# Kernel optimization log

Measured on AMD Instinct MI355X. Metric: run time of the kernel, lower is better.

The kernel has to match this reference:

```python
import jax, jax.numpy as jnp
import numpy as np

B, N, DIN, DH = 16, 512, 128, 256
NEG = -9.0e15  # matches -9000000000000000.0 in torch source


def _xavier(key, fan_in, fan_out):
    lim = float(np.sqrt(6.0 / (fan_in + fan_out)))
    return jax.random.uniform(key, (fan_in, fan_out), jnp.float32, -lim, lim)


def _l2n(x, eps=1e-12):
    # torch F.normalize: x / max(||x||, eps)
    return x / jnp.maximum(jnp.linalg.norm(x, axis=-1, keepdims=True), eps)


def _prelu(x, a):
    return jnp.where(x >= 0, x, a * x)


def setup_inputs() -> dict:
    key = jax.random.key(0)
    ks = jax.random.split(key, 12)
    seq = jax.random.normal(ks[0], (B, N, DIN), jnp.float32)
    # sparse-ish nonnegative adjacency with self loops, row-normalized
    u = jax.random.uniform(ks[1], (B, N, N), jnp.float32)
    a = jnp.where(u < 0.1, u, 0.0) + jnp.eye(N, dtype=jnp.float32)[None]
    adj = a / a.sum(-1, keepdims=True)
    # dense diffusion matrix, row-normalized
    d = jax.random.uniform(ks[2], (B, N, N), jnp.float32)
    diff = d / d.sum(-1, keepdims=True)
    # dropout keep-mask for F.dropout(p=0.1, training=True)
    keep = jax.random.bernoulli(ks[3], 0.9, (B, N, N)).astype(jnp.float32)
    drop_mask = keep / 0.9
    return {
        "seq": seq, "adj": adj, "diff": diff, "drop_mask": drop_mask,
        "fc1_w": _xavier(ks[4], DIN, DH),
        "q_w": _xavier(ks[5], DH, DH),
        "k_w": _xavier(ks[6], DH, DH),
        "v_w1": _xavier(ks[7], DH, DH),
        "v_w2": _xavier(ks[8], DH, DH),
        "fc2_w": _xavier(ks[9], DIN, DH),
        "bias1": jnp.zeros((DH,), jnp.float32),
        "bias2": jnp.zeros((DH,), jnp.float32),
        "prelu1_a": jnp.float32(0.25),
        "prelu2_a": jnp.float32(0.25),
        "v_prelu_a": jnp.float32(0.25),
    }


def reference(seq, adj, diff, drop_mask, fc1_w, q_w, k_w, v_w1, v_w2,
              fc2_w, bias1, bias2, prelu1_a, prelu2_a, v_prelu_a):
    # ---- GCN1 (attention branch) ----
    fts = seq @ fc1_w                                   # [B,N,H]
    out = jnp.einsum('bmn,bnh->bmh', adj, fts)          # adj aggregation
    q = _l2n(out @ q_w)
    k = _l2n(out @ k_w)
    scores = jax.lax.stop_gradient(jnp.einsum('bmd,bnd->bmn', q, k))  # .detach()
    div_loss = jnp.mean(jnp.sum((q - k) ** 2, axis=-1))
    att = jnp.where(adj > 0, scores, NEG)
    att = jax.nn.softmax(att, axis=-1) * drop_mask      # dropout(p=0.1)
    agg = jnp.einsum('bmn,bnh->bmh', att, out)
    v = _prelu(agg @ v_w1, v_prelu_a) @ v_w2 + bias1
    h1 = _prelu(v, prelu1_a)
    # ---- GCN2 (plain branch) ----
    h2 = _prelu(jnp.einsum('bmn,bnh->bmh', diff, seq @ fc2_w) + bias2, prelu2_a)
    # ---- Readout ----
    c1 = jnp.mean(h1, axis=1)                           # [B,H]
    c2 = jnp.mean(h2, axis=1)
    # ---- DIS ----
    n1 = _l2n(h1).reshape(B * N, DH)
    n2 = _l2n(h2).reshape(B * N, DH)
    node_logits = n1 @ n2.T                             # [B*N, B*N]
    graph_logits = _l2n(c1) @ _l2n(c2).T                # [B, B]
    return node_logits, graph_logits, div_loss
```

## Files before the change

### kernel.cpp

```cpp
#include <hip/hip_runtime.h>
#include <hip/hip_bf16.h>


using bf16x8 = __attribute__((ext_vector_type(8))) short;
using f32x4  = __attribute__((ext_vector_type(4))) float;

__device__ __forceinline__ unsigned short f2b(float f) {
    union { float f; unsigned int u; } x; x.f = f;
    unsigned int r = x.u + 0x7FFFu + ((x.u >> 16) & 1u);
    return (unsigned short)(r >> 16);
}
__device__ __forceinline__ void gload_lds16(const void* g, void* l) {
    __builtin_amdgcn_global_load_lds(
        (const __attribute__((address_space(1))) void*)g,
        (__attribute__((address_space(3))) void*)l, 16, 0, 0);
}

__global__ __launch_bounds__(256) void prep(
    const float* __restrict__ seq, const float* __restrict__ adj,
    const float* __restrict__ diff,
    const float* __restrict__ fc1, const float* __restrict__ fc2,
    const float* __restrict__ qw,  const float* __restrict__ kw,
    const float* __restrict__ v1,  const float* __restrict__ v2,
    unsigned short* __restrict__ seq_bf, unsigned short* __restrict__ adj_bf,
    unsigned short* __restrict__ diff_bf,
    unsigned short* fc1T, unsigned short* fc2T, unsigned short* qwT,
    unsigned short* kwT,  unsigned short* v1T,  unsigned short* v2T)
{
    __shared__ float t[32][33];
    const int bid = blockIdx.x, tid = threadIdx.x;
    if (bid < 9216) {
        long i = (long)bid * 256 + tid;
        const float* src; unsigned short* dst; long off;
        if (i < 262144)       { src = seq;  dst = seq_bf;  off = i; }
        else if (i < 1310720) { src = adj;  dst = adj_bf;  off = i - 262144; }
        else                  { src = diff; dst = diff_bf; off = i - 1310720; }
        float4 v = reinterpret_cast<const float4*>(src)[off];
        ushort4 o; o.x = f2b(v.x); o.y = f2b(v.y); o.z = f2b(v.z); o.w = f2b(v.w);
        reinterpret_cast<ushort4*>(dst)[off] = o;
        return;
    }
    const int r = bid - 9216;
    const int z = r >> 6;
    const float* in; unsigned short* op; int R;
    if      (z == 0) { in = fc1; op = fc1T; R = 128; }
    else if (z == 1) { in = fc2; op = fc2T; R = 128; }
    else if (z == 2) { in = qw;  op = qwT;  R = 256; }
    else if (z == 3) { in = kw;  op = kwT;  R = 256; }
    else if (z == 4) { in = v1;  op = v1T;  R = 256; }
    else             { in = v2;  op = v2T;  R = 256; }
    const int c0 = (r & 7) * 32, r0 = ((r >> 3) & 7) * 32;
    if (r0 >= R) return;
    const int x = tid & 31, y = tid >> 5;
    for (int i = 0; i < 32; i += 8) t[y + i][x] = in[(long)(r0 + y + i) * 256 + c0 + x];
    __syncthreads();
    for (int i = 0; i < 32; i += 8)
        op[(long)(c0 + y + i) * R + r0 + x] = f2b(t[x][y + i]);
}

#define BN 128
#define BK 64

template<int TBM, bool WF, bool WB, bool SWZ>
__global__ __launch_bounds__(256) void gemm_nt(
    const unsigned short* __restrict__ A, const unsigned short* __restrict__ Bt,
    float* __restrict__ Cf, unsigned short* __restrict__ Cb,
    int M, int Nn, int K, int lda, int ldb, int ldc,
    long sA, long sB, long sC)
{
    constexpr int MI = TBM / 32;
    __shared__ unsigned short As[TBM][BK];
    __shared__ unsigned short Bs[BN][BK];
    const int b = blockIdx.z;
    A  += (long)b * sA;
    Bt += (long)b * sB;
    const long cbase = (long)b * sC;

    int tx, ty;
    if (SWZ) {
        int bid = blockIdx.y * gridDim.x + blockIdx.x;
        int nwg = gridDim.x * gridDim.y;
        int cpx = nwg >> 3;
        int s = (bid & 7) * cpx + (bid >> 3);
        tx = s % gridDim.x; ty = s / gridDim.x;
    } else { tx = blockIdx.x; ty = blockIdx.y; }
    const int tile_m = ty * TBM;
    const int tile_n = tx * BN;

    const int tid  = threadIdx.x;
    const int lane = tid & 63;
    const int wave = tid >> 6;
    const int wm = (wave >> 1) * (TBM / 2);
    const int wn = (wave & 1) << 6;
    const int lrow = lane >> 3;
    const int lcol = (lane & 7) << 3;

    f32x4 acc[MI][4] = {};

    for (int k0 = 0; k0 < K; k0 += BK) {
        #pragma unroll
        for (int i = 0; i < TBM / 32; ++i) {
            const int rb = (i * 4 + wave) * 8;
            gload_lds16(A + (long)(tile_m + rb + lrow) * lda + k0 + lcol, &As[rb][0]);
        }
        #pragma unroll
        for (int i = 0; i < 4; ++i) {
            const int rb = (i * 4 + wave) * 8;
            gload_lds16(Bt + (long)(tile_n + rb + lrow) * ldb + k0 + lcol, &Bs[rb][0]);
        }
        __syncthreads();
        #pragma unroll
        for (int ks = 0; ks < 2; ++ks) {
            const int kk = ks * 32 + ((lane >> 4) << 3);
            bf16x8 af[MI], bq[4];
            #pragma unroll
            for (int mi = 0; mi < MI; ++mi)
                af[mi] = *reinterpret_cast<const bf16x8*>(&As[wm + (lane & 15) + mi * 16][kk]);
            #pragma unroll
            for (int ni = 0; ni < 4; ++ni)
                bq[ni] = *reinterpret_cast<const bf16x8*>(&Bs[wn + (lane & 15) + ni * 16][kk]);
            #pragma unroll
            for (int mi = 0; mi < MI; ++mi)
                #pragma unroll
                for (int ni = 0; ni < 4; ++ni)
                    acc[mi][ni] = __builtin_amdgcn_mfma_f32_16x16x32_bf16(
                        af[mi], bq[ni], acc[mi][ni], 0, 0, 0);
        }
        __syncthreads();
    }

    const int c0 = lane & 15;
    const int r0 = (lane >> 4) << 2;
    #pragma unroll
    for (int ni = 0; ni < 4; ++ni) {
        const int col = tile_n + wn + ni * 16 + c0;
        #pragma unroll
        for (int mi = 0; mi < MI; ++mi) {
            const int row0 = tile_m + wm + mi * 16 + r0;
            if (WF) {
                #pragma unroll
                for (int j = 0; j < 4; ++j)
                    Cf[cbase + (long)(row0 + j) * ldc + col] = acc[mi][ni][j];
            }
            if (WB) {
                #pragma unroll
                for (int j = 0; j < 4; ++j)
                    Cb[cbase + (long)(row0 + j) * ldc + col] = f2b(acc[mi][ni][j]);
            }
        }
    }
}

__global__ __launch_bounds__(256) void gcn1qk(
    const unsigned short* __restrict__ adj_bf,
    const unsigned short* __restrict__ ftsT,
    const unsigned short* __restrict__ qkT,
    unsigned short* __restrict__ outT,
    unsigned short* __restrict__ q_bf,
    unsigned short* __restrict__ k_bf)
{
    __shared__ unsigned char smem[73984];
    unsigned short* Ot  = (unsigned short*)smem;
    unsigned short* As  = (unsigned short*)(smem + 8448);
    unsigned short* Bs  = (unsigned short*)(smem + 10496);
    unsigned short* Bs2 = (unsigned short*)(smem + 8448);
    __shared__ float sred[16][4];

    const int b  = blockIdx.y;
    const int m0 = blockIdx.x << 4;
    const unsigned short* ap = adj_bf + ((long)b * 512 + m0) * 512;

    const int tid = threadIdx.x, lane = tid & 63, wave = tid >> 6;
    const int lrow = lane >> 3, lcol = (lane & 7) << 3;
    const int hi = lane >> 4, c0 = lane & 15, r0 = hi << 2;

    {
        const int wn = wave << 6;
        f32x4 acc[4] = {};
        for (int k0 = 0; k0 < 512; k0 += 64) {
            if (wave < 2)
                gload_lds16(ap + (long)(wave * 8 + lrow) * 512 + k0 + lcol, &As[wave * 8 * 64]);
            #pragma unroll
            for (int i = 0; i < 8; ++i) {
                const int rb = (i * 4 + wave) * 8;
                gload_lds16(ftsT + (long)(rb + lrow) * 8192 + b * 512 + k0 + lcol, &Bs[rb * 64]);
            }
            __syncthreads();
            #pragma unroll
            for (int ks = 0; ks < 2; ++ks) {
                const int kk = ks * 32 + (hi << 3);
                bf16x8 af = *reinterpret_cast<const bf16x8*>(&As[c0 * 64 + kk]);
                #pragma unroll
                for (int ni = 0; ni < 4; ++ni) {
                    bf16x8 bq = *reinterpret_cast<const bf16x8*>(&Bs[(wn + ni * 16 + c0) * 64 + kk]);
                    acc[ni] = __builtin_amdgcn_mfma_f32_16x16x32_bf16(af, bq, acc[ni], 0, 0, 0);
                }
            }
            __syncthreads();
        }
        #pragma unroll
        for (int ni = 0; ni < 4; ++ni) {
            const int col = wn + ni * 16 + c0;
            ushort4 o;
            unsigned short* e = (unsigned short*)&o;
            #pragma unroll
            for (int j = 0; j < 4; ++j) {
                unsigned short v = f2b(acc[ni][j]);
                e[j] = v;
                Ot[(r0 + j) * 264 + col] = v;
            }
            *reinterpret_cast<ushort4*>(
                &outT[(long)b * 131072 + (long)col * 512 + m0 + r0]) = o;
        }
    }

    {
        const int wn = wave << 7;
        f32x4 acc[8] = {};
        for (int k0 = 0; k0 < 256; k0 += 64) {
            #pragma unroll
            for (int i = 0; i < 16; ++i) {
                const int rb = (i * 4 + wave) * 8;
                gload_lds16(qkT + (long)(rb + lrow) * 256 + k0 + lcol, &Bs2[rb * 64]);
            }
            __syncthreads();
            #pragma unroll
            for (int ks = 0; ks < 2; ++ks) {
                const int kk = ks * 32 + (hi << 3);
                bf16x8 af = *reinterpret_cast<const bf16x8*>(&Ot[c0 * 264 + k0 + kk]);
                #pragma unroll
                for (int ni = 0; ni < 8; ++ni) {
                    bf16x8 bq = *reinterpret_cast<const bf16x8*>(&Bs2[(wn + ni * 16 + c0) * 64 + kk]);
                    acc[ni] = __builtin_amdgcn_mfma_f32_16x16x32_bf16(af, bq, acc[ni], 0, 0, 0);
                }
            }
            __syncthreads();
        }
        float rs[4] = {};
        #pragma unroll
        for (int ni = 0; ni < 8; ++ni)
            #pragma unroll
            for (int j = 0; j < 4; ++j) { float x = acc[ni][j]; rs[j] += x * x; }
        #pragma unroll
        for (int o = 1; o <= 8; o <<= 1)
            #pragma unroll
            for (int j = 0; j < 4; ++j) rs[j] += __shfl_xor(rs[j], o);
        if (c0 == 0) {
            #pragma unroll
            for (int j = 0; j < 4; ++j) sred[r0 + j][wave] = rs[j];
        }
        __syncthreads();
        float inv[4];
        #pragma unroll
        for (int j = 0; j < 4; ++j) {
            const int rr = r0 + j;
            float sq = sred[rr][0] + sred[rr][1];
            float sk = sred[rr][2] + sred[rr][3];
            inv[j] = 1.f / fmaxf(sqrtf(wave < 2 ? sq : sk), 1e-12f);
        }
        #pragma unroll
        for (int ni = 0; ni < 8; ++ni)
            #pragma unroll
            for (int j = 0; j < 4; ++j) {
                const long rowg = (long)b * 512 + m0 + r0 + j;
                const int col = wn + ni * 16 + c0;
                unsigned short v = f2b(acc[ni][j] * inv[j]);
                if (wave < 2) q_bf[rowg * 256 + col] = v;
                else          k_bf[rowg * 256 + col - 256] = v;
            }
    }
}

__global__ __launch_bounds__(256) void attmlp_h2(
    const unsigned short* __restrict__ q_bf,
    const unsigned short* __restrict__ k_bf,
    const unsigned short* __restrict__ adj_bf,
    const float* __restrict__ drop,
    const unsigned short* __restrict__ outT,
    const unsigned short* __restrict__ w1T,
    const unsigned short* __restrict__ w2T,
    const float* __restrict__ bias1,
    const float* __restrict__ av, const float* __restrict__ a1,
    unsigned short* __restrict__ n1,
    float* __restrict__ psum1,
    float* __restrict__ rowpart,
    const unsigned short* __restrict__ diff_bf,
    const unsigned short* __restrict__ fts2T,
    const float* __restrict__ bias2, const float* __restrict__ a2,
    unsigned short* __restrict__ n2,
    float* __restrict__ psum2)
{
    __shared__ unsigned char smem[69632];
    __shared__ float redm[32][4], reds[32][4];

    const int idx = blockIdx.x >> 1;
    const int tid = threadIdx.x, lane = tid & 63, wave = tid >> 6;
    const int lrow = lane >> 3, lcol = (lane & 7) << 3;
    const int hi = lane >> 4, c0 = lane & 15, r0 = hi << 2;

    if (blockIdx.x & 1) {
        unsigned short* As  = (unsigned short*)smem;
        unsigned short* Bs  = (unsigned short*)(smem + 4096);
        unsigned short* Pls = (unsigned short*)smem;
        unsigned short* Bs2 = (unsigned short*)(smem + 34816);
        unsigned short* T   = (unsigned short*)smem;
        unsigned short* Bs3 = (unsigned short*)(smem + 16896);

        const int b  = idx >> 4;
        const int m0 = (idx & 15) << 5;
        const unsigned short* qp = q_bf + (long)b * 131072 + (long)m0 * 256;
        const unsigned short* kp = k_bf + (long)b * 131072;
        const unsigned short* ot = outT + (long)b * 131072;
        const unsigned short* ap = adj_bf + ((long)b * 512 + m0) * 512;
        const float*          dp = drop   + ((long)b * 512 + m0) * 512;

        {
            const int wn = wave << 7;
            f32x4 acc[2][8] = {};
            for (int k0 = 0; k0 < 256; k0 += 64) {
                gload_lds16(qp + (long)(wave * 8 + lrow) * 256 + k0 + lcol, &As[wave * 8 * 64]);
                #pragma unroll
                for (int i = 0; i < 16; ++i) {
                    const int rb = (i * 4 + wave) * 8;
                    gload_lds16(kp + (long)(rb + lrow) * 256 + k0 + lcol, &Bs[rb * 64]);
                }
                __syncthreads();
                #pragma unroll
                for (int ks = 0; ks < 2; ++ks) {
                    const int kk = ks * 32 + (hi << 3);
                    bf16x8 af[2], bq[8];
                    #pragma unroll
                    for (int mi = 0; mi < 2; ++mi)
                        af[mi] = *reinterpret_cast<const bf16x8*>(&As[(mi * 16 + c0) * 64 + kk]);
                    #pragma unroll
                    for (int ni = 0; ni < 8; ++ni)
                        bq[ni] = *reinterpret_cast<const bf16x8*>(&Bs[(wn + ni * 16 + c0) * 64 + kk]);
                    #pragma unroll
                    for (int mi = 0; mi < 2; ++mi)
                        #pragma unroll
                        for (int ni = 0; ni < 8; ++ni)
                            acc[mi][ni] = __builtin_amdgcn_mfma_f32_16x16x32_bf16(
                                af[mi], bq[ni], acc[mi][ni], 0, 0, 0);
                }
                __syncthreads();
            }

            float rmax[2][4];
            #pragma unroll
            for (int mi = 0; mi < 2; ++mi)
                #pragma unroll
                for (int j = 0; j < 4; ++j) rmax[mi][j] = -3.0e38f;
            #pragma unroll
            for (int mi = 0; mi < 2; ++mi)
                #pragma unroll
                for (int ni = 0; ni < 8; ++ni)
                    #pragma unroll
                    for (int j = 0; j < 4; ++j) {
                        const int rowl = mi * 16 + r0 + j;
                        const int col  = wn + ni * 16 + c0;
                        float s = acc[mi][ni][j];
                        if (col == m0 + rowl)
                            rowpart[(long)b * 512 + m0 + rowl] = 2.f - 2.f * s;
                        bool m = ap[(long)rowl * 512 + col] != 0;
                        s = m ? s : -3.0e38f;
                        acc[mi][ni][j] = s;
                        rmax[mi][j] = fmaxf(rmax[mi][j], s);
                    }
            #pragma unroll
            for (int o = 1; o <= 8; o <<= 1)
                #pragma unroll
                for (int mi = 0; mi < 2; ++mi)
                    #pragma unroll
                    for (int j = 0; j < 4; ++j)
                        rmax[mi][j] = fmaxf(rmax[mi][j], __shfl_xor(rmax[mi][j], o));
            if (c0 == 0) {
                #pragma unroll
                for (int mi = 0; mi < 2; ++mi)
                    #pragma unroll
                    for (int j = 0; j < 4; ++j) redm[mi * 16 + r0 + j][wave] = rmax[mi][j];
            }
            __syncthreads();
            float mx[2][4], rsum[2][4];
            #pragma unroll
            for (int mi = 0; mi < 2; ++mi)
                #pragma unroll
                for (int j = 0; j < 4; ++j) {
                    const int rr = mi * 16 + r0 + j;
                    mx[mi][j] = fmaxf(fmaxf(redm[rr][0], redm[rr][1]),
                                      fmaxf(redm[rr][2], redm[rr][3]));
                    rsum[mi][j] = 0.f;
                }
            #pragma unroll
            for (int mi = 0; mi < 2; ++mi)
                #pragma unroll
                for (int ni = 0; ni < 8; ++ni)
                    #pragma unroll
                    for (int j = 0; j < 4; ++j) {
                        float e = __expf(acc[mi][ni][j] - mx[mi][j]);
                        acc[mi][ni][j] = e;
                        rsum[mi][j] += e;
                    }
            #pragma unroll
            for (int o = 1; o <= 8; o <<= 1)
                #pragma unroll
                for (int mi = 0; mi < 2; ++mi)
                    #pragma unroll
                    for (int j = 0; j < 4; ++j) rsum[mi][j] += __shfl_xor(rsum[mi][j], o);
            if (c0 == 0) {
                #pragma unroll
                for (int mi = 0; mi < 2; ++mi)
                    #pragma unroll
                    for (int j = 0; j < 4; ++j) reds[mi * 16 + r0 + j][wave] = rsum[mi][j];
            }
            __syncthreads();
            float inv[2][4];
            #pragma unroll
            for (int mi = 0; mi < 2; ++mi)
                #pragma unroll
                for (int j = 0; j < 4; ++j) {
                    const int rr = mi * 16 + r0 + j;
                    inv[mi][j] = 1.f / (reds[rr][0] + reds[rr][1] + reds[rr][2] + reds[rr][3]);
                }
            #pragma unroll
            for (int mi = 0; mi < 2; ++mi)
                #pragma unroll
                for (int ni = 0; ni < 8; ++ni)
                    #pragma unroll
                    for (int j = 0; j < 4; ++j) {
                        const int rowl = mi * 16 + r0 + j;
                        const int col  = wn + ni * 16 + c0;
                        float p = acc[mi][ni][j] * inv[mi][j] * dp[(long)rowl * 512 + col];
                        Pls[rowl * 520 + col] = f2b(p);
                    }
        }
        __syncthreads();

        f32x4 acc2[2][4] = {};
        {
            const int wn = wave << 6;
            for (int k0 = 0; k0 < 512; k0 += 64) {
                #pragma unroll
                for (int i = 0; i < 8; ++i) {
                    const int rb = (i * 4 + wave) * 8;
                    gload_lds16(ot + (long)(rb + lrow) * 512 + k0 + lcol, &Bs2[rb * 64]);
                }
                __syncthreads();
                #pragma unroll
                for (int ks = 0; ks < 2; ++ks) {
                    const int kk = ks * 32 + (hi << 3);
                    bf16x8 af[2], bq[4];
                    #pragma unroll
                    for (int mi = 0; mi < 2; ++mi)
                        af[mi] = *reinterpret_cast<const bf16x8*>(&Pls[(mi * 16 + c0) * 520 + k0 + kk]);
                    #pragma unroll
                    for (int ni = 0; ni < 4; ++ni)
                        bq[ni] = *reinterpret_cast<const bf16x8*>(&Bs2[(wn + ni * 16 + c0) * 64 + kk]);
                    #pragma unroll
                    for (int mi = 0; mi < 2; ++mi)
                        #pragma unroll
                        for (int ni = 0; ni < 4; ++ni)
                            acc2[mi][ni] = __builtin_amdgcn_mfma_f32_16x16x32_bf16(
                                af[mi], bq[ni], acc2[mi][ni], 0, 0, 0);
                }
                __syncthreads();
            }
        }

        const int wn6 = wave << 6;
        const float alphav = av[0];
        #pragma unroll
        for (int mi = 0; mi < 2; ++mi)
            #pragma unroll
            for (int ni = 0; ni < 4; ++ni)
                #pragma unroll
                for (int j = 0; j < 4; ++j)
                    T[(mi * 16 + r0 + j) * 264 + wn6 + ni * 16 + c0] = f2b(acc2[mi][ni][j]);
        f32x4 acct[2][4] = {};
        for (int k0 = 0; k0 < 256; k0 += 64) {
            #pragma unroll
            for (int i = 0; i < 8; ++i) {
                const int rb = (i * 4 + wave) * 8;
                gload_lds16(w1T + (long)(rb + lrow) * 256 + k0 + lcol, &Bs3[rb * 64]);
            }
            __syncthreads();
            #pragma unroll
            for (int ks = 0; ks < 2; ++ks) {
                const int kk = ks * 32 + (hi << 3);
                bf16x8 af[2], bq[4];
                #pragma unroll
                for (int mi = 0; mi < 2; ++mi)
                    af[mi] = *reinterpret_cast<const bf16x8*>(&T[(mi * 16 + c0) * 264 + k0 + kk]);
                #pragma unroll
                for (int ni = 0; ni < 4; ++ni)
                    bq[ni] = *reinterpret_cast<const bf16x8*>(&Bs3[(wn6 + ni * 16 + c0) * 64 + kk]);
                #pragma unroll
                for (int mi = 0; mi < 2; ++mi)
                    #pragma unroll
                    for (int ni = 0; ni < 4; ++ni)
                        acct[mi][ni] = __builtin_amdgcn_mfma_f32_16x16x32_bf16(
                            af[mi], bq[ni], acct[mi][ni], 0, 0, 0);
            }
            __syncthreads();
        }
        #pragma unroll
        for (int mi = 0; mi < 2; ++mi)
            #pragma unroll
            for (int ni = 0; ni < 4; ++ni)
                #pragma unroll
                for (int j = 0; j < 4; ++j) {
                    float x = acct[mi][ni][j];
                    x = (x >= 0.f) ? x : alphav * x;
                    T[(mi * 16 + r0 + j) * 264 + wn6 + ni * 16 + c0] = f2b(x);
                }

        f32x4 acc3[2][4] = {};
        for (int k0 = 0; k0 < 256; k0 += 64) {
            #pragma unroll
            for (int i = 0; i < 8; ++i) {
                const int rb = (i * 4 + wave) * 8;
                gload_lds16(w2T + (long)(rb + lrow) * 256 + k0 + lcol, &Bs3[rb * 64]);
            }
            __syncthreads();
            #pragma unroll
            for (int ks = 0; ks < 2; ++ks) {
                const int kk = ks * 32 + (hi << 3);
                bf16x8 af[2], bq[4];
                #pragma unroll
                for (int mi = 0; mi < 2; ++mi)
                    af[mi] = *reinterpret_cast<const bf16x8*>(&T[(mi * 16 + c0) * 264 + k0 + kk]);
                #pragma unroll
                for (int ni = 0; ni < 4; ++ni)
                    bq[ni] = *reinterpret_cast<const bf16x8*>(&Bs3[(wn6 + ni * 16 + c0) * 64 + kk]);
                #pragma unroll
                for (int mi = 0; mi < 2; ++mi)
                    #pragma unroll
                    for (int ni = 0; ni < 4; ++ni)
                        acc3[mi][ni] = __builtin_amdgcn_mfma_f32_16x16x32_bf16(
                            af[mi], bq[ni], acc3[mi][ni], 0, 0, 0);
            }
            __syncthreads();
        }

        const float alpha1 = a1[0];
        float rs[2][4] = {};
        #pragma unroll
        for (int ni = 0; ni < 4; ++ni) {
            const float bv = bias1[wn6 + ni * 16 + c0];
            #pragma unroll
            for (int mi = 0; mi < 2; ++mi)
                #pragma unroll
                for (int j = 0; j < 4; ++j) {
                    float x = acc3[mi][ni][j] + bv;
                    x = (x >= 0.f) ? x : alpha1 * x;
                    acc3[mi][ni][j] = x;
                    rs[mi][j] += x * x;
                }
        }
        #pragma unroll
        for (int o = 1; o <= 8; o <<= 1)
            #pragma unroll
            for (int mi = 0; mi < 2; ++mi)
                #pragma unroll
                for (int j = 0; j < 4; ++j) rs[mi][j] += __shfl_xor(rs[mi][j], o);
        if (c0 == 0) {
            #pragma unroll
            for (int mi = 0; mi < 2; ++mi)
                #pragma unroll
                for (int j = 0; j < 4; ++j) redm[mi * 16 + r0 + j][wave] = rs[mi][j];
        }
        __syncthreads();
        float inv2[2][4];
        #pragma unroll
        for (int mi = 0; mi < 2; ++mi)
            #pragma unroll
            for (int j = 0; j < 4; ++j) {
                const int rr = mi * 16 + r0 + j;
                float s = redm[rr][0] + redm[rr][1] + redm[rr][2] + redm[rr][3];
                inv2[mi][j] = 1.f / fmaxf(sqrtf(s), 1e-12f);
            }
        float cs[4];
        #pragma unroll
        for (int ni = 0; ni < 4; ++ni) {
            float s = 0.f;
            #pragma unroll
            for (int mi = 0; mi < 2; ++mi)
                #pragma unroll
                for (int j = 0; j < 4; ++j) s += acc3[mi][ni][j];
            s += __shfl_xor(s, 16);
            s += __shfl_xor(s, 32);
            cs[ni] = s;
        }
        if (lane < 16) {
            #pragma unroll
            for (int ni = 0; ni < 4; ++ni)
                psum1[(long)idx * 256 + wn6 + ni * 16 + lane] = cs[ni];
        }
        const long row0g = (long)b * 512 + m0;
        #pragma unroll
        for (int mi = 0; mi < 2; ++mi)
            #pragma unroll
            for (int ni = 0; ni < 4; ++ni)
                #pragma unroll
                for (int j = 0; j < 4; ++j)
                    n1[(row0g + mi * 16 + r0 + j) * 256 + wn6 + ni * 16 + c0] =
                        f2b(acc3[mi][ni][j] * inv2[mi][j]);
    } else {
        unsigned short* As = (unsigned short*)smem;
        unsigned short* Bs = (unsigned short*)(smem + 4096);

        const int z = idx >> 4;
        const int arow0 = (idx & 15) << 5;
        const unsigned short* A = diff_bf + (long)z * 262144;
        const unsigned short* Bt = fts2T + z * 512;
        const int wn = wave << 6;

        f32x4 acc[2][4] = {};
        for (int k0 = 0; k0 < 512; k0 += 64) {
            {
                const int rb = wave * 8;
                gload_lds16(A + (long)(arow0 + rb + lrow) * 512 + k0 + lcol, &As[rb * 64]);
            }
            #pragma unroll
            for (int i = 0; i < 8; ++i) {
                const int rb = (i * 4 + wave) * 8;
                gload_lds16(Bt + (long)(rb + lrow) * 8192 + k0 + lcol, &Bs[rb * 64]);
            }
            __syncthreads();
            #pragma unroll
            for (int ks = 0; ks < 2; ++ks) {
                const int kk = ks * 32 + (hi << 3);
                bf16x8 af[2], bq[4];
                #pragma unroll
                for (int mi = 0; mi < 2; ++mi)
                    af[mi] = *reinterpret_cast<const bf16x8*>(&As[(mi * 16 + c0) * 64 + kk]);
                #pragma unroll
                for (int ni = 0; ni < 4; ++ni)
                    bq[ni] = *reinterpret_cast<const bf16x8*>(&Bs[(wn + ni * 16 + c0) * 64 + kk]);
                #pragma unroll
                for (int mi = 0; mi < 2; ++mi)
                    #pragma unroll
                    for (int ni = 0; ni < 4; ++ni)
                        acc[mi][ni] = __builtin_amdgcn_mfma_f32_16x16x32_bf16(
                            af[mi], bq[ni], acc[mi][ni], 0, 0, 0);
            }
            __syncthreads();
        }

        const float alpha = a2[0];
        float rs[2][4] = {};
        #pragma unroll
        for (int ni = 0; ni < 4; ++ni) {
            const float bv = bias2[wn + ni * 16 + c0];
            #pragma unroll
            for (int mi = 0; mi < 2; ++mi)
                #pragma unroll
                for (int j = 0; j < 4; ++j) {
                    float x = acc[mi][ni][j] + bv;
                    x = (x >= 0.f) ? x : alpha * x;
                    acc[mi][ni][j] = x;
                    rs[mi][j] += x * x;
                }
        }
        #pragma unroll
        for (int o = 1; o <= 8; o <<= 1)
            #pragma unroll
            for (int mi = 0; mi < 2; ++mi)
                #pragma unroll
                for (int j = 0; j < 4; ++j) rs[mi][j] += __shfl_xor(rs[mi][j], o);
        if (c0 == 0) {
            #pragma unroll
            for (int mi = 0; mi < 2; ++mi)
                #pragma unroll
                for (int j = 0; j < 4; ++j) redm[mi * 16 + r0 + j][wave] = rs[mi][j];
        }
        __syncthreads();
        float inv[2][4];
        #pragma unroll
        for (int mi = 0; mi < 2; ++mi)
            #pragma unroll
            for (int j = 0; j < 4; ++j) {
                const int rr = mi * 16 + r0 + j;
                float s = redm[rr][0] + redm[rr][1] + redm[rr][2] + redm[rr][3];
                inv[mi][j] = 1.f / fmaxf(sqrtf(s), 1e-12f);
            }
        float cs[4];
        #pragma unroll
        for (int ni = 0; ni < 4; ++ni) {
            float s = 0.f;
            #pragma unroll
            for (int mi = 0; mi < 2; ++mi)
                #pragma unroll
                for (int j = 0; j < 4; ++j) s += acc[mi][ni][j];
            s += __shfl_xor(s, 16);
            s += __shfl_xor(s, 32);
            cs[ni] = s;
        }
        if (lane < 16) {
            #pragma unroll
            for (int ni = 0; ni < 4; ++ni)
                psum2[(long)idx * 256 + wn + ni * 16 + lane] = cs[ni];
        }
        const long grow0 = (long)idx * 32;
        #pragma unroll
        for (int mi = 0; mi < 2; ++mi)
            #pragma unroll
            for (int ni = 0; ni < 4; ++ni)
                #pragma unroll
                for (int j = 0; j < 4; ++j)
                    n2[(grow0 + mi * 16 + r0 + j) * 256 + wn + ni * 16 + c0] =
                        f2b(acc[mi][ni][j] * inv[mi][j]);
    }
}

__global__ __launch_bounds__(256) void creduce(const float* __restrict__ psum1,
                                               const float* __restrict__ psum2,
                                               float* __restrict__ c1n,
                                               float* __restrict__ c2n) {
    const int which = blockIdx.x & 1, g = blockIdx.x >> 1;
    const float* ps = which ? psum2 : psum1;
    float* cn = which ? c2n : c1n;
    const int t = threadIdx.x;
    float s = 0.f;
    #pragma unroll
    for (int c = 0; c < 16; ++c) s += ps[(long)(g * 16 + c) * 256 + t];
    s *= (1.f / 512.f);
    float ss = s * s;
    #pragma unroll
    for (int o = 32; o; o >>= 1) ss += __shfl_xor(ss, o);
    __shared__ float red[4];
    if ((t & 63) == 0) red[t >> 6] = ss;
    __syncthreads();
    float tot = red[0] + red[1] + red[2] + red[3];
    cn[g * 256 + t] = s / fmaxf(sqrtf(tot), 1e-12f);
}

__global__ __launch_bounds__(256) void graphf3(const float* __restrict__ c1n,
                                               const float* __restrict__ c2n,
                                               const float* __restrict__ rowpart,
                                               float* __restrict__ out_g,
                                               float* __restrict__ out_div) {
    const int t = threadIdx.x, ii = t >> 4, jj = t & 15;
    float s = 0.f;
    for (int h = 0; h < 256; ++h) s += c1n[ii * 256 + h] * c2n[jj * 256 + h];
    out_g[ii * 16 + jj] = s;
    float ds = 0.f;
    for (int i = t; i < 8192; i += 256) ds += rowpart[i];
    #pragma unroll
    for (int o = 32; o; o >>= 1) ds += __shfl_xor(ds, o);
    __shared__ float red[4];
    if ((t & 63) == 0) red[t >> 6] = ds;
    __syncthreads();
    if (t == 0) out_div[0] = (red[0] + red[1] + red[2] + red[3]) * (1.f / 8192.f);
}

static constexpr long OFF_SEQ_BF  = 0;
static constexpr long OFF_FC1T    = 2097152;
static constexpr long OFF_QWT     = 2228224;
static constexpr long OFF_VW1T    = 2490368;
static constexpr long OFF_VW2T    = 2621440;
static constexpr long OFF_ADJ     = 3145728;
static constexpr long OFF_DIFF    = 11534336;
static constexpr long OFF_FTST    = 19922944;
static constexpr long OFF_OUTT    = 28311552;
static constexpr long OFF_QBF     = 32505856;
static constexpr long OFF_KBF     = 36700160;
static constexpr long OFF_N1      = 40894464;
static constexpr long OFF_N2      = 45088768;
static constexpr long OFF_PSUM    = 49283072;
static constexpr long OFF_ROWPART = 49807360;
static constexpr long OFF_C1N     = 49840128;
static constexpr long OFF_C2N     = 49856512;

extern "C" void kernel_launch(void* const* d_in, const int* in_sizes, int n_in,
                              void* d_out, int out_size, void* d_ws, size_t ws_size,
                              hipStream_t stream) {
    const float* seq      = (const float*)d_in[0];
    const float* adj      = (const float*)d_in[1];
    const float* diff     = (const float*)d_in[2];
    const float* drop     = (const float*)d_in[3];
    const float* fc1_w    = (const float*)d_in[4];
    const float* q_w      = (const float*)d_in[5];
    const float* k_w      = (const float*)d_in[6];
    const float* v_w1     = (const float*)d_in[7];
    const float* v_w2     = (const float*)d_in[8];
    const float* fc2_w    = (const float*)d_in[9];
    const float* bias1    = (const float*)d_in[10];
    const float* bias2    = (const float*)d_in[11];
    const float* prelu1_a = (const float*)d_in[12];
    const float* prelu2_a = (const float*)d_in[13];
    const float* v_prelu  = (const float*)d_in[14];
    float* out = (float*)d_out;

    char* ws = (char*)d_ws;
    unsigned short* seq_bf  = (unsigned short*)(ws + OFF_SEQ_BF);
    unsigned short* fc1T    = (unsigned short*)(ws + OFF_FC1T);
    unsigned short* fc2T    = (unsigned short*)(ws + OFF_FC1T + 65536);
    unsigned short* qwT     = (unsigned short*)(ws + OFF_QWT);
    unsigned short* kwT     = (unsigned short*)(ws + OFF_QWT + 131072);
    unsigned short* vw1T    = (unsigned short*)(ws + OFF_VW1T);
    unsigned short* vw2T    = (unsigned short*)(ws + OFF_VW2T);
    unsigned short* adj_bf  = (unsigned short*)(ws + OFF_ADJ);
    unsigned short* diff_bf = (unsigned short*)(ws + OFF_DIFF);
    unsigned short* ftsT    = (unsigned short*)(ws + OFF_FTST);
    unsigned short* fts2T   = (unsigned short*)(ws + OFF_FTST + 4194304);
    unsigned short* outT    = (unsigned short*)(ws + OFF_OUTT);
    unsigned short* q_bf    = (unsigned short*)(ws + OFF_QBF);
    unsigned short* k_bf    = (unsigned short*)(ws + OFF_KBF);
    unsigned short* n1_bf   = (unsigned short*)(ws + OFF_N1);
    unsigned short* n2_bf   = (unsigned short*)(ws + OFF_N2);
    float*          psum1   = (float*)(ws + OFF_PSUM);
    float*          psum2   = (float*)(ws + OFF_PSUM + 262144);
    float*          rowpart = (float*)(ws + OFF_ROWPART);
    float*          c1n     = (float*)(ws + OFF_C1N);
    float*          c2n     = (float*)(ws + OFF_C2N);

    prep<<<9600, 256, 0, stream>>>(seq, adj, diff, fc1_w, fc2_w, q_w, k_w, v_w1, v_w2,
                                   seq_bf, adj_bf, diff_bf, fc1T, fc2T, qwT, kwT, vw1T, vw2T);

    gemm_nt<64, false, true, false><<<dim3(64, 4, 2), 256, 0, stream>>>(
        fc1T, seq_bf, nullptr, ftsT,
        256, 8192, 128, 128, 128, 8192, 32768, 0, 2097152);

    gcn1qk<<<dim3(32, 16), 256, 0, stream>>>(adj_bf, ftsT, qwT, outT, q_bf, k_bf);

    attmlp_h2<<<512, 256, 0, stream>>>(
        q_bf, k_bf, adj_bf, drop, outT, vw1T, vw2T, bias1, v_prelu, prelu1_a,
        n1_bf, psum1, rowpart,
        diff_bf, fts2T, bias2, prelu2_a, n2_bf, psum2);

    creduce<<<32, 256, 0, stream>>>(psum1, psum2, c1n, c2n);
    graphf3<<<1, 256, 0, stream>>>(c1n, c2n, rowpart, out + 67108864, out + 67109120);

    gemm_nt<128, true, false, true><<<dim3(64, 64, 1), 256, 0, stream>>>(
        n1_bf, n2_bf, out, nullptr,
        8192, 8192, 256, 256, 256, 8192, 0, 0, 0);

    (void)in_sizes; (void)n_in; (void)out_size; (void)ws_size;
}
```

Measured before the change: 212.6 us.

## Stage fp32 GEMM output through LDS for coalesced nontemporal stores; fuse readout kernels

The final 8192x8192 fp32 node-logits GEMM now writes its accumulators into a shared-memory bounce buffer, reusing the A/B tile space, in two half-tile passes. It then emits 16-byte row-contiguous nontemporal stores instead of scattered 4-byte stores, aiming to cut write-transaction overhead on the 256MB output. Separately, the creduce and graphf3 kernels are merged into a single-block readout kernel, removing one launch and the intermediate normalized buffers. The change adds extra barriers and LDS traffic in the epilogue, and the merged readout does its reduction serially in one block.

```diff
diff --git a/kernel.cpp b/kernel.cpp
--- a/kernel.cpp
+++ b/kernel.cpp
@@ -69,8 +69,9 @@
     long sA, long sB, long sC)
 {
     constexpr int MI = TBM / 32;
-    __shared__ unsigned short As[TBM][BK];
-    __shared__ unsigned short Bs[BN][BK];
+    __shared__ unsigned char smem_g[(TBM + BN) * BK * 2];
+    unsigned short* As = (unsigned short*)smem_g;
+    unsigned short* Bs = (unsigned short*)(smem_g + TBM * BK * 2);
     const int b = blockIdx.z;
     A  += (long)b * sA;
     Bt += (long)b * sB;
@@ -101,12 +102,12 @@
         #pragma unroll
         for (int i = 0; i < TBM / 32; ++i) {
             const int rb = (i * 4 + wave) * 8;
-            gload_lds16(A + (long)(tile_m + rb + lrow) * lda + k0 + lcol, &As[rb][0]);
+            gload_lds16(A + (long)(tile_m + rb + lrow) * lda + k0 + lcol, &As[rb * BK]);
         }
         #pragma unroll
         for (int i = 0; i < 4; ++i) {
             const int rb = (i * 4 + wave) * 8;
-            gload_lds16(Bt + (long)(tile_n + rb + lrow) * ldb + k0 + lcol, &Bs[rb][0]);
+            gload_lds16(Bt + (long)(tile_n + rb + lrow) * ldb + k0 + lcol, &Bs[rb * BK]);
         }
         __syncthreads();
         #pragma unroll
@@ -115,10 +116,10 @@
             bf16x8 af[MI], bq[4];
             #pragma unroll
             for (int mi = 0; mi < MI; ++mi)
-                af[mi] = *reinterpret_cast<const bf16x8*>(&As[wm + (lane & 15) + mi * 16][kk]);
+                af[mi] = *reinterpret_cast<const bf16x8*>(&As[(wm + (lane & 15) + mi * 16) * BK + kk]);
             #pragma unroll
             for (int ni = 0; ni < 4; ++ni)
-                bq[ni] = *reinterpret_cast<const bf16x8*>(&Bs[wn + (lane & 15) + ni * 16][kk]);
+                bq[ni] = *reinterpret_cast<const bf16x8*>(&Bs[(wn + (lane & 15) + ni * 16) * BK + kk]);
             #pragma unroll
             for (int mi = 0; mi < MI; ++mi)
                 #pragma unroll
@@ -131,21 +132,44 @@
 
     const int c0 = lane & 15;
     const int r0 = (lane >> 4) << 2;
-    #pragma unroll
-    for (int ni = 0; ni < 4; ++ni) {
-        const int col = tile_n + wn + ni * 16 + c0;
-        #pragma unroll
-        for (int mi = 0; mi < MI; ++mi) {
-            const int row0 = tile_m + wm + mi * 16 + r0;
-            if (WF) {
-                #pragma unroll
-                for (int j = 0; j < 4; ++j)
-                    Cf[cbase + (long)(row0 + j) * ldc + col] = acc[mi][ni][j];
-            }
-            if (WB) {
+
+    if (WB) {
+        #pragma unroll
+        for (int ni = 0; ni < 4; ++ni) {
+            const int col = tile_n + wn + ni * 16 + c0;
+            #pragma unroll
+            for (int mi = 0; mi < MI; ++mi) {
+                const int row0 = tile_m + wm + mi * 16 + r0;
                 #pragma unroll
                 for (int j = 0; j < 4; ++j)
                     Cb[cbase + (long)(row0 + j) * ldc + col] = f2b(acc[mi][ni][j]);
+            }
+        }
+    }
+    if (WF) {
+        float* bounce = (float*)smem_g;
+        const int tr = tid >> 5;
+        const int tc = (tid & 31) << 2;
+        #pragma unroll
+        for (int h = 0; h < 2; ++h) {
+            __syncthreads();
+            if ((wave >> 1) == h) {
+                #pragma unroll
+                for (int mi = 0; mi < MI; ++mi)
+                    #pragma unroll
+                    for (int ni = 0; ni < 4; ++ni)
+                        #pragma unroll
+                        for (int j = 0; j < 4; ++j)
+                            bounce[(mi * 16 + r0 + j) * 128 + wn + ni * 16 + c0] =
+                                acc[mi][ni][j];
+            }
+            __syncthreads();
+            #pragma unroll
+            for (int p = 0; p < 8; ++p) {
+                const int rl = p * 8 + tr;
+                f32x4 v = *reinterpret_cast<const f32x4*>(&bounce[rl * 128 + tc]);
+                __builtin_nontemporal_store(v, reinterpret_cast<f32x4*>(
+                    &Cf[cbase + (long)(tile_m + h * 64 + rl) * ldc + tile_n + tc]));
             }
         }
     }
@@ -712,37 +736,36 @@
     }
 }
 
-__global__ __launch_bounds__(256) void creduce(const float* __restrict__ psum1,
-                                               const float* __restrict__ psum2,
-                                               float* __restrict__ c1n,
-                                               float* __restrict__ c2n) {
-    const int which = blockIdx.x & 1, g = blockIdx.x >> 1;
-    const float* ps = which ? psum2 : psum1;
-    float* cn = which ? c2n : c1n;
+__global__ __launch_bounds__(256) void readout(
+    const float* __restrict__ psum1, const float* __restrict__ psum2,
+    const float* __restrict__ rowpart,
+    float* __restrict__ out_g, float* __restrict__ out_div)
+{
+    __shared__ float c1s[16][256], c2s[16][256];
+    __shared__ float invn[32];
     const int t = threadIdx.x;
+    for (int g = 0; g < 16; ++g) {
+        float s1 = 0.f, s2 = 0.f;
+        #pragma unroll
+        for (int c = 0; c < 16; ++c) {
+            s1 += psum1[(long)(g * 16 + c) * 256 + t];
+            s2 += psum2[(long)(g * 16 + c) * 256 + t];
+        }
+        c1s[g][t] = s1 * (1.f / 512.f);
+        c2s[g][t] = s2 * (1.f / 512.f);
+    }
+    __syncthreads();
+    if (t < 32) {
+        const float* row = (t < 16) ? c1s[t] : c2s[t - 16];
+        float ss = 0.f;
+        for (int h = 0; h < 256; ++h) { float v = row[h]; ss += v * v; }
+        invn[t] = 1.f / fmaxf(sqrtf(ss), 1e-12f);
+    }
+    __syncthreads();
+    const int ii = t >> 4, jj = t & 15;
     float s = 0.f;
-    #pragma unroll
-    for (int c = 0; c < 16; ++c) s += ps[(long)(g * 16 + c) * 256 + t];
-    s *= (1.f / 512.f);
-    float ss = s * s;
-    #pragma unroll
-    for (int o = 32; o; o >>= 1) ss += __shfl_xor(ss, o);
-    __shared__ float red[4];
-    if ((t & 63) == 0) red[t >> 6] = ss;
-    __syncthreads();
-    float tot = red[0] + red[1] + red[2] + red[3];
-    cn[g * 256 + t] = s / fmaxf(sqrtf(tot), 1e-12f);
-}
-
-__global__ __launch_bounds__(256) void graphf3(const float* __restrict__ c1n,
-                                               const float* __restrict__ c2n,
-                                               const float* __restrict__ rowpart,
-                                               float* __restrict__ out_g,
-                                               float* __restrict__ out_div) {
-    const int t = threadIdx.x, ii = t >> 4, jj = t & 15;
-    float s = 0.f;
-    for (int h = 0; h < 256; ++h) s += c1n[ii * 256 + h] * c2n[jj * 256 + h];
-    out_g[ii * 16 + jj] = s;
+    for (int h = 0; h < 256; ++h) s += c1s[ii][h] * c2s[jj][h];
+    out_g[ii * 16 + jj] = s * invn[ii] * invn[16 + jj];
     float ds = 0.f;
     for (int i = t; i < 8192; i += 256) ds += rowpart[i];
     #pragma unroll
@@ -768,8 +791,6 @@
 static constexpr long OFF_N2      = 45088768;
 static constexpr long OFF_PSUM    = 49283072;
 static constexpr long OFF_ROWPART = 49807360;
-static constexpr long OFF_C1N     = 49840128;
-static constexpr long OFF_C2N     = 49856512;
 
 extern "C" void kernel_launch(void* const* d_in, const int* in_sizes, int n_in,
                               void* d_out, int out_size, void* d_ws, size_t ws_size,
@@ -811,8 +832,6 @@
     float*          psum1   = (float*)(ws + OFF_PSUM);
     float*          psum2   = (float*)(ws + OFF_PSUM + 262144);
     float*          rowpart = (float*)(ws + OFF_ROWPART);
-    float*          c1n     = (float*)(ws + OFF_C1N);
-    float*          c2n     = (float*)(ws + OFF_C2N);
 
     prep<<<9600, 256, 0, stream>>>(seq, adj, diff, fc1_w, fc2_w, q_w, k_w, v_w1, v_w2,
                                    seq_bf, adj_bf, diff_bf, fc1T, fc2T, qwT, kwT, vw1T, vw2T);
@@ -828,8 +847,7 @@
         n1_bf, psum1, rowpart,
         diff_bf, fts2T, bias2, prelu2_a, n2_bf, psum2);
 
-    creduce<<<32, 256, 0, stream>>>(psum1, psum2, c1n, c2n);
-    graphf3<<<1, 256, 0, stream>>>(c1n, c2n, rowpart, out + 67108864, out + 67109120);
+    readout<<<1, 256, 0, stream>>>(psum1, psum2, rowpart, out + 67108864, out + 67109120);
 
     gemm_nt<128, true, false, true><<<dim3(64, 64, 1), 256, 0, stream>>>(
         n1_bf, n2_bf, out, nullptr,
```

Result: faster. 206.1 us (-3.1%).
